# Optimization experiments

Hardware: AMD Instinct MI355X
Metric: run time of the kernel (lower is better)

## Reference

```python
import jax, jax.numpy as jnp
import numpy as np

N_NODES = 100000
N_EDGES = 1600000
IN_DIM = 10
HID = 64
OUT_DIM = 2


def _gcn_norm(edge_index, num_nodes):
    # PyG gcn_norm with add_self_loops=False, edge_weight=1
    src, dst = edge_index[0], edge_index[1]
    deg = jnp.zeros((num_nodes,), jnp.float32).at[dst].add(1.0)
    dinv = jnp.where(deg > 0, jax.lax.rsqrt(deg), 0.0)
    return dinv[src] * dinv[dst]  # [E]


def _arma_conv(x, edge_index, norm, W, V, b):
    # ARMAConv, num_stacks=1, num_layers=1 (PyG defaults):
    # out = A_norm @ (x @ W_init) + x @ V_root + b   (no internal act at T=1)
    src, dst = edge_index[0], edge_index[1]
    h = x @ W                                   # [N, F_out]
    msg = norm[:, None] * h[src]                # [E, F_out] gather
    agg = jax.ops.segment_sum(msg, dst, num_segments=x.shape[0])  # scatter-add
    return agg + x @ V + b


def setup_inputs() -> dict:
    key = jax.random.key(0)
    ks = jax.random.split(key, 9)
    x = jax.random.uniform(ks[0], (N_NODES, IN_DIM), dtype=jnp.float32)
    edge_index = jax.random.randint(ks[1], (2, N_EDGES), 0, N_NODES, dtype=jnp.int64)
    s = 0.1
    W1 = jax.random.normal(ks[2], (IN_DIM, HID), jnp.float32) * s
    V1 = jax.random.normal(ks[3], (IN_DIM, HID), jnp.float32) * s
    b1 = jnp.zeros((HID,), jnp.float32)
    W2 = jax.random.normal(ks[4], (HID, HID), jnp.float32) * s
    V2 = jax.random.normal(ks[5], (HID, HID), jnp.float32) * s
    b2 = jnp.zeros((HID,), jnp.float32)
    W3 = jax.random.normal(ks[6], (HID, OUT_DIM), jnp.float32) * s
    V3 = jax.random.normal(ks[7], (HID, OUT_DIM), jnp.float32) * s
    b3 = jnp.zeros((OUT_DIM,), jnp.float32)
    return {"x": x, "edge_index": edge_index,
            "W1": W1, "V1": V1, "b1": b1,
            "W2": W2, "V2": V2, "b2": b2,
            "W3": W3, "V3": V3, "b3": b3}


def reference(x, edge_index, W1, V1, b1, W2, V2, b2, W3, V3, b3):
    norm = _gcn_norm(edge_index, x.shape[0])
    h = jax.nn.relu(_arma_conv(x, edge_index, norm, W1, V1, b1))
    # dropout is identity at eval time
    h = jax.nn.relu(_arma_conv(h, edge_index, norm, W2, V2, b2))
    h = _arma_conv(h, edge_index, norm, W3, V3, b3)
    return jax.nn.log_softmax(h, axis=1)
```

## Files before the change

kernel.cpp:

```cpp
#include <hip/hip_runtime.h>
#include <hip/hip_fp16.h>
#include <math.h>

#define NN 100000
#define NE 1600000
#define HID 64
#define BN 128
#define NBUCK 782
#define FBCAP 2304
#define NSB 49
#define SBCAP 34816
#define CHUNK1 2048
#define NBLK1 782
#define NSLICE 16
#define SLCAP 2304
#define CSTRIDE 32
#define XPITCH 136

typedef _Float16 half8 __attribute__((ext_vector_type(8)));
typedef float floatx4 __attribute__((ext_vector_type(4)));

__device__ __forceinline__ __half2 shfl_xor_h2(__half2 v, int m) {
    unsigned int u = *(unsigned int*)&v;
    u = __shfl_xor(u, m);
    return *(__half2*)&u;
}
__device__ __forceinline__ unsigned int h2bits(__half2 v) {
    return *(unsigned int*)&v;
}


__global__ __launch_bounds__(256) void k_binA1(const int* __restrict__ src,
                                               const int* __restrict__ dst,
                                               int* __restrict__ bcur1,
                                               unsigned int* __restrict__ sbdata) {
    __shared__ unsigned int par[CHUNK1];
    __shared__ unsigned short rnk[CHUNK1];
    __shared__ unsigned char bkt[CHUNK1];
    __shared__ int hist[NSB];
    __shared__ int base[NSB];
    int tid = threadIdx.x;
    int e0 = blockIdx.x * CHUNK1;
    int m = NE - e0; if (m > CHUNK1) m = CHUNK1;
    if (tid < NSB) hist[tid] = 0;
    __syncthreads();
    for (int i = tid; i < m; i += 256) {
        int s = src[e0 + i], d = dst[e0 + i];
        int b = d >> 11;
        par[i] = (unsigned int)s | ((unsigned int)(d & 2047) << 17);
        bkt[i] = (unsigned char)b;
        rnk[i] = (unsigned short)atomicAdd(&hist[b], 1);
    }
    __syncthreads();
    if (tid < NSB) {
        int h = hist[tid];
        base[tid] = h ? atomicAdd(&bcur1[tid * CSTRIDE], h) : 0;
    }
    __syncthreads();
    for (int i = tid; i < m; i += 256) {
        int b = bkt[i];
        int pos = base[b] + rnk[i];
        if (pos < SBCAP) sbdata[(size_t)b * SBCAP + pos] = par[i];
    }
}

__global__ __launch_bounds__(256) void k_binA2(const int* __restrict__ bcur1,
                                               const unsigned int* __restrict__ sbdata,
                                               int* __restrict__ bcur2,
                                               unsigned int* __restrict__ fbdata) {
    __shared__ unsigned int par[SLCAP];
    __shared__ unsigned short rnk[SLCAP];
    __shared__ unsigned char bkt[SLCAP];
    __shared__ int hist[16];
    __shared__ int base[16];
    int tid = threadIdx.x;
    int sb = blockIdx.x >> 4, sl = blockIdx.x & 15;
    int m = bcur1[sb * CSTRIDE]; if (m > SBCAP) m = SBCAP;
    int L = (m + NSLICE - 1) >> 4;
    int lo = sl * L;
    int cnt = m - lo; if (cnt > L) cnt = L; if (cnt < 0) cnt = 0;
    if (tid < 16) hist[tid] = 0;
    __syncthreads();
    const unsigned int* sp = sbdata + (size_t)sb * SBCAP + lo;
    for (int i = tid; i < cnt; i += 256) {
        unsigned int u = sp[i];
        int dlow = (u >> 17) & 2047;
        int f = dlow >> 7;
        par[i] = (u & 0x1ffffu) | ((unsigned int)(dlow & 127) << 17);
        bkt[i] = (unsigned char)f;
        rnk[i] = (unsigned short)atomicAdd(&hist[f], 1);
    }
    __syncthreads();
    if (tid < 16) {
        int h = hist[tid];
        base[tid] = h ? atomicAdd(&bcur2[(sb * 16 + tid) * CSTRIDE], h) : 0;
    }
    __syncthreads();
    for (int i = tid; i < cnt; i += 256) {
        int f = bkt[i];
        int pos = base[f] + rnk[i];
        if (pos < FBCAP) fbdata[(size_t)(sb * 16 + f) * FBCAP + pos] = par[i];
    }
}

__global__ void k_bscan(const int* __restrict__ bcur2, int* __restrict__ ebase) {
    __shared__ int ls[16];
    int t = threadIdx.x;
    int lane = t & 63, wid = t >> 6;
    int v = 0;
    if (t < NBUCK) {
        int m = bcur2[t * CSTRIDE];
        v = (m < FBCAP) ? m : FBCAP;
    }
    int orig = v;
    for (int off = 1; off < 64; off <<= 1) {
        int u = __shfl_up(v, off);
        if (lane >= off) v += u;
    }
    if (lane == 63) ls[wid] = v;
    __syncthreads();
    if (wid == 0) {
        int w = (lane < 16) ? ls[lane] : 0;
        for (int off = 1; off < 16; off <<= 1) {
            int u = __shfl_up(w, off);
            if (lane >= off) w += u;
        }
        if (lane < 16) ls[lane] = w;
    }
    __syncthreads();
    int base = wid ? ls[wid - 1] : 0;
    int incl = base + v;
    if (t < NBUCK) ebase[t] = incl - orig;
    if (t == NBUCK - 1) ebase[NBUCK] = incl;
}

__global__ __launch_bounds__(256) void k_binB(const int* __restrict__ bcur2,
                                              const int* __restrict__ ebase,
                                              const unsigned int* __restrict__ fbdata,
                                              int* __restrict__ rp, float* __restrict__ dinv,
                                              int* __restrict__ perm) {
    __shared__ unsigned int se[FBCAP];
    __shared__ int cnt[BN];
    __shared__ int scn[BN];
    int b = blockIdx.x, tid = threadIdx.x;
    int m = bcur2[b * CSTRIDE]; if (m > FBCAP) m = FBCAP;
    int base = ebase[b];
    for (int i = tid; i < m; i += 256) se[i] = fbdata[(size_t)b * FBCAP + i];
    if (tid < BN) cnt[tid] = 0;
    __syncthreads();
    for (int i = tid; i < m; i += 256) atomicAdd(&cnt[se[i] >> 17], 1);
    __syncthreads();
    int c = (tid < BN) ? cnt[tid] : 0;
    int g = b * BN + tid;
    if (tid < BN && g < NN) dinv[g] = (c > 0) ? rsqrtf((float)c) : 0.0f;
    if (tid < BN) scn[tid] = c;
    __syncthreads();
    for (int off = 1; off < BN; off <<= 1) {
        int u = (tid >= off && tid < BN) ? scn[tid - off] : 0;
        __syncthreads();
        if (tid < BN) scn[tid] += u;
        __syncthreads();
    }
    if (tid < BN) {
        int excl = scn[tid] - c;
        if (g < NN) rp[g] = base + excl;
        cnt[tid] = excl;
    }
    if (b == NBUCK - 1 && tid == 0) rp[NN] = ebase[NBUCK];
    __syncthreads();
    for (int i = tid; i < m; i += 256) {
        unsigned int u = se[i];
        int pos = atomicAdd(&cnt[u >> 17], 1);
        perm[base + pos] = (int)(u & 0x1ffffu);
    }
}


__global__ __launch_bounds__(256) void k_l1f(
        const int* __restrict__ rp, const int* __restrict__ perm,
        const float* __restrict__ dinv, const float* __restrict__ x,
        const float* __restrict__ W, const float* __restrict__ V,
        const float* __restrict__ b, unsigned short* __restrict__ th, int N) {
    __shared__ float sW[640], sV[640];
    for (int i = threadIdx.x; i < 640; i += 256) { sW[i] = W[i]; sV[i] = V[i]; }
    __syncthreads();
    int n = (blockIdx.x * 256 + threadIdx.x) >> 4;
    if (n >= N) return;
    int sub = threadIdx.x & 15;
    int beg = rp[n], end = rp[n + 1];
    float ag[10];
#pragma unroll
    for (int k = 0; k < 10; ++k) ag[k] = 0.0f;
    for (int j = beg + sub; j < end; j += 16) {
        int s = perm[j];
        float w = dinv[s];
        const float2* xr = (const float2*)(x + (size_t)s * 10);
        float2 v0 = xr[0], v1 = xr[1], v2 = xr[2], v3 = xr[3], v4 = xr[4];
        ag[0] += w * v0.x; ag[1] += w * v0.y; ag[2] += w * v1.x; ag[3] += w * v1.y;
        ag[4] += w * v2.x; ag[5] += w * v2.y; ag[6] += w * v3.x; ag[7] += w * v3.y;
        ag[8] += w * v4.x; ag[9] += w * v4.y;
    }
#pragma unroll
    for (int mk = 1; mk <= 8; mk <<= 1) {
#pragma unroll
        for (int k = 0; k < 10; ++k) ag[k] += __shfl_xor(ag[k], mk);
    }
    float dn = dinv[n];
#pragma unroll
    for (int k = 0; k < 10; ++k) ag[k] *= dn;
    const float2* xn = (const float2*)(x + (size_t)n * 10);
    float2 x0 = xn[0], x1 = xn[1], x2 = xn[2], x3 = xn[3], x4 = xn[4];
    float xv[10] = {x0.x, x0.y, x1.x, x1.y, x2.x, x2.y, x3.x, x3.y, x4.x, x4.y};
    int f0 = sub * 4;
    float4 bb = *(const float4*)(b + f0);
    float acc[4] = {bb.x, bb.y, bb.z, bb.w};
#pragma unroll
    for (int k = 0; k < 10; ++k) {
        float4 wq = *(const float4*)&sW[k * HID + f0];
        float4 vq = *(const float4*)&sV[k * HID + f0];
        acc[0] += ag[k] * wq.x + xv[k] * vq.x;
        acc[1] += ag[k] * wq.y + xv[k] * vq.y;
        acc[2] += ag[k] * wq.z + xv[k] * vq.z;
        acc[3] += ag[k] * wq.w + xv[k] * vq.w;
    }
    __half2 lo = __floats2half2_rn(fmaxf(acc[0], 0.0f), fmaxf(acc[1], 0.0f));
    __half2 hi = __floats2half2_rn(fmaxf(acc[2], 0.0f), fmaxf(acc[3], 0.0f));
    *(uint2*)(th + (size_t)n * HID + f0) = make_uint2(h2bits(lo), h2bits(hi));
}


__global__ __launch_bounds__(256) void k_agg64h(
        const int* __restrict__ rp, const int* __restrict__ perm,
        const float* __restrict__ dinv, const unsigned short* __restrict__ th,
        unsigned short* __restrict__ aggth, int N) {
    int wid = (blockIdx.x * blockDim.x + threadIdx.x) >> 6;
    if (wid >= N) return;
    int n = __builtin_amdgcn_readfirstlane(wid);
    int lane = threadIdx.x & 63;
    int grp = lane >> 3;
    int sub = lane & 7;
    int beg = rp[n], end = rp[n + 1];
    __half2 a0 = __float2half2_rn(0.0f), a1 = a0, a2 = a0, a3 = a0;
    for (int j = beg + grp; j < end; j += 8) {
        int s = perm[j];
        __half2 w2 = __float2half2_rn(dinv[s]);
        uint4 u = *(const uint4*)(th + (size_t)s * HID + sub * 8);
        a0 = __hfma2(w2, *(__half2*)&u.x, a0);
        a1 = __hfma2(w2, *(__half2*)&u.y, a1);
        a2 = __hfma2(w2, *(__half2*)&u.z, a2);
        a3 = __hfma2(w2, *(__half2*)&u.w, a3);
    }
#pragma unroll
    for (int m = 8; m < 64; m <<= 1) {
        a0 = __hadd2(a0, shfl_xor_h2(a0, m));
        a1 = __hadd2(a1, shfl_xor_h2(a1, m));
        a2 = __hadd2(a2, shfl_xor_h2(a2, m));
        a3 = __hadd2(a3, shfl_xor_h2(a3, m));
    }
    if (grp == 0) {
        __half2 dn2 = __float2half2_rn(dinv[n]);
        uint4 o;
        o.x = h2bits(__hmul2(dn2, a0));
        o.y = h2bits(__hmul2(dn2, a1));
        o.z = h2bits(__hmul2(dn2, a2));
        o.w = h2bits(__hmul2(dn2, a3));
        *(uint4*)(aggth + (size_t)n * HID + sub * 8) = o;
    }
}

__global__ __launch_bounds__(256) void k_agg3lsm(const int* __restrict__ rp,
                                                 const int* __restrict__ perm,
                                                 const float* __restrict__ dinv,
                                                 const float2* __restrict__ h3,
                                                 const float2* __restrict__ y3,
                                                 float* __restrict__ out, int N) {
    int n = (blockIdx.x * 256 + threadIdx.x) >> 4;
    if (n >= N) return;
    int sl = threadIdx.x & 15;
    int beg = rp[n], end = rp[n + 1];
    float a0 = 0.0f, a1 = 0.0f;
    for (int j = beg + sl; j < end; j += 16) {
        int s = perm[j];
        float w = dinv[s];
        float2 hh = h3[s];
        a0 += w * hh.x;
        a1 += w * hh.y;
    }
#pragma unroll
    for (int mk = 1; mk <= 8; mk <<= 1) {
        a0 += __shfl_xor(a0, mk);
        a1 += __shfl_xor(a1, mk);
    }
    if (sl == 0) {
        float dn = dinv[n];
        float2 yy = y3[n];
        float z0 = dn * a0 + yy.x;
        float z1 = dn * a1 + yy.y;
        float m = fmaxf(z0, z1);
        float l = m + logf(expf(z0 - m) + expf(z1 - m));
        out[n * 2 + 0] = z0 - l;
        out[n * 2 + 1] = z1 - l;
    }
}


__global__ __launch_bounds__(256) void k_dense23m(
        const unsigned short* __restrict__ aggth, const unsigned short* __restrict__ th,
        const float* __restrict__ W, const float* __restrict__ V,
        const float* __restrict__ b, const float* __restrict__ W3,
        const float* __restrict__ V3, const float* __restrict__ b3,
        float2* __restrict__ h3, float2* __restrict__ y3, int N) {
    __shared__ _Float16 sX[64 * XPITCH];
    __shared__ _Float16 sWT[64 * XPITCH];
    __shared__ float sB2[64];
    __shared__ float sW3[128], sV3[128];
    int tid = threadIdx.x;
    int base = blockIdx.x * 64;
    {
        int f = tid & 63;
        int g = tid >> 6;
        const float* Wsrc = (g < 2) ? W : V;
        int kbase = (g & 1) * 32;
        int Kbase = (g < 2) ? kbase : (64 + kbase);
#pragma unroll
        for (int k2 = 0; k2 < 32; k2 += 2) {
            float w0 = Wsrc[(kbase + k2) * 64 + f];
            float w1 = Wsrc[(kbase + k2 + 1) * 64 + f];
            __half2 h = __floats2half2_rn(w0, w1);
            *(unsigned int*)&sWT[f * XPITCH + Kbase + k2] = h2bits(h);
        }
        if (tid < 64) sB2[tid] = b[tid];
        if (tid < 128) { sW3[tid] = W3[tid]; sV3[tid] = V3[tid]; }
    }
    {
        int n = tid >> 2, p = tid & 3;
        int g = base + n;
        uint4 z = make_uint4(0, 0, 0, 0);
        uint4 a0 = z, a1 = z, c0 = z, c1 = z;
        if (g < N) {
            const uint4* ap = (const uint4*)(aggth + (size_t)g * HID + p * 16);
            const uint4* cp = (const uint4*)(th + (size_t)g * HID + p * 16);
            a0 = ap[0]; a1 = ap[1];
            c0 = cp[0]; c1 = cp[1];
        }
        *(uint4*)&sX[n * XPITCH + p * 16] = a0;
        *(uint4*)&sX[n * XPITCH + p * 16 + 8] = a1;
        *(uint4*)&sX[n * XPITCH + 64 + p * 16] = c0;
        *(uint4*)&sX[n * XPITCH + 64 + p * 16 + 8] = c1;
    }
    __syncthreads();
    int lane = tid & 63;
    int wv = tid >> 6;
    int ml = lane & 15, quad = lane >> 4;
    half8 a[4];
#pragma unroll
    for (int kt = 0; kt < 4; ++kt)
        a[kt] = *(const half8*)&sX[(wv * 16 + ml) * XPITCH + kt * 32 + quad * 8];
    float p0[4] = {}, p1[4] = {}, q0[4] = {}, q1[4] = {};
#pragma unroll
    for (int c = 0; c < 4; ++c) {
        floatx4 acc = {0.0f, 0.0f, 0.0f, 0.0f};
#pragma unroll
        for (int kt = 0; kt < 4; ++kt) {
            half8 bf = *(const half8*)&sWT[(c * 16 + ml) * XPITCH + kt * 32 + quad * 8];
            acc = __builtin_amdgcn_mfma_f32_16x16x32_f16(a[kt], bf, acc, 0, 0, 0);
        }
        int col = c * 16 + ml;
        float bias = sB2[col];
        float w30 = sW3[col * 2], w31 = sW3[col * 2 + 1];
        float v30 = sV3[col * 2], v31 = sV3[col * 2 + 1];
#pragma unroll
        for (int r = 0; r < 4; ++r) {
            float t = fmaxf(acc[r] + bias, 0.0f);
            p0[r] += t * w30; p1[r] += t * w31;
            q0[r] += t * v30; q1[r] += t * v31;
        }
    }
#pragma unroll
    for (int mk = 1; mk <= 8; mk <<= 1) {
#pragma unroll
        for (int r = 0; r < 4; ++r) {
            p0[r] += __shfl_xor(p0[r], mk);
            p1[r] += __shfl_xor(p1[r], mk);
            q0[r] += __shfl_xor(q0[r], mk);
            q1[r] += __shfl_xor(q1[r], mk);
        }
    }
    if (ml == 0) {
        float b30 = b3[0], b31 = b3[1];
#pragma unroll
        for (int r = 0; r < 4; ++r) {
            int g = base + wv * 16 + quad * 4 + r;
            if (g < N) {
                h3[g] = make_float2(p0[r], p1[r]);
                y3[g] = make_float2(q0[r] + b30, q1[r] + b31);
            }
        }
    }
}


extern "C" void kernel_launch(void* const* d_in, const int* in_sizes, int n_in,
                              void* d_out, int out_size, void* d_ws, size_t ws_size,
                              hipStream_t stream) {
    const float* x  = (const float*)d_in[0];
    const int*   ei = (const int*)d_in[1];
    const int*   src = ei;
    const int*   dst = ei + NE;
    const float* W1 = (const float*)d_in[2];
    const float* V1 = (const float*)d_in[3];
    const float* b1 = (const float*)d_in[4];
    const float* W2 = (const float*)d_in[5];
    const float* V2 = (const float*)d_in[6];
    const float* b2 = (const float*)d_in[7];
    const float* W3 = (const float*)d_in[8];
    const float* V3 = (const float*)d_in[9];
    const float* b3 = (const float*)d_in[10];
    float* out = (float*)d_out;

    float* ws = (float*)d_ws;
    int*   bcur1 = (int*)ws;
    int*   bcur2 = (int*)(ws + 2048);
    int*   ebase = (int*)(ws + 27136);
    int*   rp    = (int*)(ws + 28160);
    float* dinv  = ws + 128512;
    unsigned int* sbdata = (unsigned int*)(ws + 228864);
    int*   perm  = (int*)(ws + 228864);
    unsigned int* fbdata = (unsigned int*)(ws + 1934848);
    float2* h3   = (float2*)(ws + 1934848);
    float2* y3   = (float2*)(ws + 1934848 + 2 * NN);
    unsigned short* aggth = (unsigned short*)(ws + 8334848);
    unsigned short* th    = (unsigned short*)(ws + 14734848);

    const int B = 256;

    hipMemsetAsync(bcur1, 0, 27072 * sizeof(int), stream);
    k_binA1<<<NBLK1, B, 0, stream>>>(src, dst, bcur1, sbdata);
    k_binA2<<<NSB * NSLICE, B, 0, stream>>>(bcur1, sbdata, bcur2, fbdata);
    k_bscan<<<1, 1024, 0, stream>>>(bcur2, ebase);
    k_binB<<<NBUCK, B, 0, stream>>>(bcur2, ebase, fbdata, rp, dinv, perm);

    k_l1f<<<(NN * 16 + B - 1) / B, B, 0, stream>>>(rp, perm, dinv, x, W1, V1, b1, th, NN);

    k_agg64h<<<(NN * 64 + B - 1) / B, B, 0, stream>>>(rp, perm, dinv, th, aggth, NN);
    k_dense23m<<<(NN + 63) / 64, B, 0, stream>>>(aggth, th, W2, V2, b2, W3, V3, b3,
                                                 h3, y3, NN);

    k_agg3lsm<<<(NN * 16 + B - 1) / B, B, 0, stream>>>(rp, perm, dinv,
                                                       (const float2*)h3,
                                                       (const float2*)y3, out, NN);
}
```

Baseline: 224.9 us.

## Pack quantized source dinv into perm entries and unroll 64-wide aggregation

Adds a pass that stores each edge's source dinv as a 15-bit fixed-point value in the upper bits of the perm index. The three aggregation kernels then decode the weight from the packed word instead of doing a dependent random gather of dinv[src]. The 64-wide aggregation loop is also unrolled by two to keep more loads in flight, and the binning chunk size is doubled with half as many blocks. This costs an extra full-edge kernel pass and quantizes dinv to about 6e-5 resolution, which adds precision error; values of 2 or more would overflow the 15-bit field.

Result: faster. 219.2 us (-2.5%).

```diff
diff --git a/kernel.cpp b/kernel.cpp
--- a/kernel.cpp
+++ b/kernel.cpp
@@ -10,8 +10,8 @@
 #define FBCAP 2304
 #define NSB 49
 #define SBCAP 34816
-#define CHUNK1 2048
-#define NBLK1 782
+#define CHUNK1 4096
+#define NBLK1 391
 #define NSLICE 16
 #define SLCAP 2304
 #define CSTRIDE 32
@@ -27,6 +27,9 @@
 }
 __device__ __forceinline__ unsigned int h2bits(__half2 v) {
     return *(unsigned int*)&v;
+}
+__device__ __forceinline__ float wdec(unsigned int u) {
+    return (float)(u >> 17) * 6.103515625e-05f;
 }
 
 
@@ -175,9 +178,19 @@
     }
 }
 
+__global__ __launch_bounds__(256) void k_wpack(int* __restrict__ perm,
+                                               const float* __restrict__ dinv, int E) {
+    int i = blockIdx.x * blockDim.x + threadIdx.x;
+    if (i < E) {
+        unsigned int s = (unsigned int)perm[i];
+        int q = __float2int_rn(dinv[s] * 16384.0f);
+        perm[i] = (int)(s | ((unsigned int)q << 17));
+    }
+}
+
 
 __global__ __launch_bounds__(256) void k_l1f(
-        const int* __restrict__ rp, const int* __restrict__ perm,
+        const int* __restrict__ rp, const unsigned int* __restrict__ pw,
         const float* __restrict__ dinv, const float* __restrict__ x,
         const float* __restrict__ W, const float* __restrict__ V,
         const float* __restrict__ b, unsigned short* __restrict__ th, int N) {
@@ -192,8 +205,9 @@
 #pragma unroll
     for (int k = 0; k < 10; ++k) ag[k] = 0.0f;
     for (int j = beg + sub; j < end; j += 16) {
-        int s = perm[j];
-        float w = dinv[s];
+        unsigned int pe = pw[j];
+        int s = pe & 0x1ffff;
+        float w = wdec(pe);
         const float2* xr = (const float2*)(x + (size_t)s * 10);
         float2 v0 = xr[0], v1 = xr[1], v2 = xr[2], v3 = xr[3], v4 = xr[4];
         ag[0] += w * v0.x; ag[1] += w * v0.y; ag[2] += w * v1.x; ag[3] += w * v1.y;
@@ -230,7 +244,7 @@
 
 
 __global__ __launch_bounds__(256) void k_agg64h(
-        const int* __restrict__ rp, const int* __restrict__ perm,
+        const int* __restrict__ rp, const unsigned int* __restrict__ pw,
         const float* __restrict__ dinv, const unsigned short* __restrict__ th,
         unsigned short* __restrict__ aggth, int N) {
     int wid = (blockIdx.x * blockDim.x + threadIdx.x) >> 6;
@@ -241,14 +255,32 @@
     int sub = lane & 7;
     int beg = rp[n], end = rp[n + 1];
     __half2 a0 = __float2half2_rn(0.0f), a1 = a0, a2 = a0, a3 = a0;
-    for (int j = beg + grp; j < end; j += 8) {
-        int s = perm[j];
-        __half2 w2 = __float2half2_rn(dinv[s]);
-        uint4 u = *(const uint4*)(th + (size_t)s * HID + sub * 8);
-        a0 = __hfma2(w2, *(__half2*)&u.x, a0);
-        a1 = __hfma2(w2, *(__half2*)&u.y, a1);
-        a2 = __hfma2(w2, *(__half2*)&u.z, a2);
-        a3 = __hfma2(w2, *(__half2*)&u.w, a3);
+    int j = beg + grp;
+    for (; j + 8 < end; j += 16) {
+        unsigned int pa = pw[j], pb = pw[j + 8];
+        int sa = pa & 0x1ffff, sb = pb & 0x1ffff;
+        __half2 wa = __float2half2_rn(wdec(pa));
+        __half2 wb = __float2half2_rn(wdec(pb));
+        uint4 ua = *(const uint4*)(th + (size_t)sa * HID + sub * 8);
+        uint4 ub = *(const uint4*)(th + (size_t)sb * HID + sub * 8);
+        a0 = __hfma2(wa, *(__half2*)&ua.x, a0);
+        a1 = __hfma2(wa, *(__half2*)&ua.y, a1);
+        a2 = __hfma2(wa, *(__half2*)&ua.z, a2);
+        a3 = __hfma2(wa, *(__half2*)&ua.w, a3);
+        a0 = __hfma2(wb, *(__half2*)&ub.x, a0);
+        a1 = __hfma2(wb, *(__half2*)&ub.y, a1);
+        a2 = __hfma2(wb, *(__half2*)&ub.z, a2);
+        a3 = __hfma2(wb, *(__half2*)&ub.w, a3);
+    }
+    if (j < end) {
+        unsigned int pa = pw[j];
+        int sa = pa & 0x1ffff;
+        __half2 wa = __float2half2_rn(wdec(pa));
+        uint4 ua = *(const uint4*)(th + (size_t)sa * HID + sub * 8);
+        a0 = __hfma2(wa, *(__half2*)&ua.x, a0);
+        a1 = __hfma2(wa, *(__half2*)&ua.y, a1);
+        a2 = __hfma2(wa, *(__half2*)&ua.z, a2);
+        a3 = __hfma2(wa, *(__half2*)&ua.w, a3);
     }
 #pragma unroll
     for (int m = 8; m < 64; m <<= 1) {
@@ -269,7 +301,7 @@
 }
 
 __global__ __launch_bounds__(256) void k_agg3lsm(const int* __restrict__ rp,
-                                                 const int* __restrict__ perm,
+                                                 const unsigned int* __restrict__ pw,
                                                  const float* __restrict__ dinv,
                                                  const float2* __restrict__ h3,
                                                  const float2* __restrict__ y3,
@@ -280,8 +312,9 @@
     int beg = rp[n], end = rp[n + 1];
     float a0 = 0.0f, a1 = 0.0f;
     for (int j = beg + sl; j < end; j += 16) {
-        int s = perm[j];
-        float w = dinv[s];
+        unsigned int pe = pw[j];
+        int s = pe & 0x1ffff;
+        float w = wdec(pe);
         float2 hh = h3[s];
         a0 += w * hh.x;
         a1 += w * hh.y;
@@ -439,14 +472,17 @@
     k_binA2<<<NSB * NSLICE, B, 0, stream>>>(bcur1, sbdata, bcur2, fbdata);
     k_bscan<<<1, 1024, 0, stream>>>(bcur2, ebase);
     k_binB<<<NBUCK, B, 0, stream>>>(bcur2, ebase, fbdata, rp, dinv, perm);
-
-    k_l1f<<<(NN * 16 + B - 1) / B, B, 0, stream>>>(rp, perm, dinv, x, W1, V1, b1, th, NN);
-
-    k_agg64h<<<(NN * 64 + B - 1) / B, B, 0, stream>>>(rp, perm, dinv, th, aggth, NN);
+    k_wpack<<<(NE + B - 1) / B, B, 0, stream>>>(perm, dinv, NE);
+
+    k_l1f<<<(NN * 16 + B - 1) / B, B, 0, stream>>>(rp, (const unsigned int*)perm,
+                                                   dinv, x, W1, V1, b1, th, NN);
+
+    k_agg64h<<<(NN * 64 + B - 1) / B, B, 0, stream>>>(rp, (const unsigned int*)perm,
+                                                      dinv, th, aggth, NN);
     k_dense23m<<<(NN + 63) / 64, B, 0, stream>>>(aggth, th, W2, V2, b2, W3, V3, b3,
                                                  h3, y3, NN);
 
-    k_agg3lsm<<<(NN * 16 + B - 1) / B, B, 0, stream>>>(rp, perm, dinv,
-                                                       (const float2*)h3,
+    k_agg3lsm<<<(NN * 16 + B - 1) / B, B, 0, stream>>>(rp, (const unsigned int*)perm,
+                                                       dinv, (const float2*)h3,
                                                        (const float2*)y3, out, NN);
 }
```

## Pre-scale node features by source degree norm to drop per-edge dinv gathers

Applied to the files above, without the earlier changes.

Moves the dinv[src] factor out of every edge loop by storing pre-scaled copies of node features (y = dinv*x, th2 = dinv*h, h3 scaled by dinv), so each aggregation only sums gathered rows. binB now records each edge's rank in its destination during the first atomic pass and uses a shuffle-based scan, removing the second atomic pass and the shared-memory scan loop. The 64-wide aggregation is unrolled by two, and the first binning kernel uses larger chunks with fewer blocks. In exchange it writes extra buffers (th2, y) and, because fp16 values are now scaled per node before summation, changes rounding.

Measured after the change: 212.3 us. -5.6%, faster.

```diff
diff --git a/kernel.cpp b/kernel.cpp
--- a/kernel.cpp
+++ b/kernel.cpp
@@ -10,8 +10,8 @@
 #define FBCAP 2304
 #define NSB 49
 #define SBCAP 34816
-#define CHUNK1 2048
-#define NBLK1 782
+#define CHUNK1 4096
+#define NBLK1 391
 #define NSLICE 16
 #define SLCAP 2304
 #define CSTRIDE 32
@@ -138,40 +138,64 @@
                                               const int* __restrict__ ebase,
                                               const unsigned int* __restrict__ fbdata,
                                               int* __restrict__ rp, float* __restrict__ dinv,
-                                              int* __restrict__ perm) {
+                                              int* __restrict__ perm,
+                                              const float* __restrict__ x,
+                                              float* __restrict__ y) {
     __shared__ unsigned int se[FBCAP];
+    __shared__ unsigned short rnk[FBCAP];
     __shared__ int cnt[BN];
-    __shared__ int scn[BN];
+    __shared__ int ex[BN];
+    __shared__ float sdv[BN];
+    __shared__ int wsum[2];
     int b = blockIdx.x, tid = threadIdx.x;
     int m = bcur2[b * CSTRIDE]; if (m > FBCAP) m = FBCAP;
     int base = ebase[b];
-    for (int i = tid; i < m; i += 256) se[i] = fbdata[(size_t)b * FBCAP + i];
     if (tid < BN) cnt[tid] = 0;
     __syncthreads();
-    for (int i = tid; i < m; i += 256) atomicAdd(&cnt[se[i] >> 17], 1);
-    __syncthreads();
-    int c = (tid < BN) ? cnt[tid] : 0;
-    int g = b * BN + tid;
-    if (tid < BN && g < NN) dinv[g] = (c > 0) ? rsqrtf((float)c) : 0.0f;
-    if (tid < BN) scn[tid] = c;
-    __syncthreads();
-    for (int off = 1; off < BN; off <<= 1) {
-        int u = (tid >= off && tid < BN) ? scn[tid - off] : 0;
-        __syncthreads();
-        if (tid < BN) scn[tid] += u;
-        __syncthreads();
-    }
+    for (int i = tid; i < m; i += 256) {
+        unsigned int u = fbdata[(size_t)b * FBCAP + i];
+        se[i] = u;
+        rnk[i] = (unsigned short)atomicAdd(&cnt[u >> 17], 1);
+    }
+    __syncthreads();
     if (tid < BN) {
-        int excl = scn[tid] - c;
+        int c = cnt[tid];
+        int v = c;
+        int lane = tid & 63;
+        for (int off = 1; off < 64; off <<= 1) {
+            int u = __shfl_up(v, off);
+            if (lane >= off) v += u;
+        }
+        if (lane == 63) wsum[tid >> 6] = v;
+        int g = b * BN + tid;
+        float dv = (c > 0) ? rsqrtf((float)c) : 0.0f;
+        sdv[tid] = dv;
+        if (g < NN) dinv[g] = dv;
+        cnt[tid] = v - c;
+    }
+    __syncthreads();
+    if (tid < BN) {
+        int excl = cnt[tid] + ((tid >= 64) ? wsum[0] : 0);
+        ex[tid] = excl;
+        int g = b * BN + tid;
         if (g < NN) rp[g] = base + excl;
-        cnt[tid] = excl;
     }
     if (b == NBUCK - 1 && tid == 0) rp[NN] = ebase[NBUCK];
     __syncthreads();
     for (int i = tid; i < m; i += 256) {
         unsigned int u = se[i];
-        int pos = atomicAdd(&cnt[u >> 17], 1);
-        perm[base + pos] = (int)(u & 0x1ffffu);
+        int dl = u >> 17;
+        perm[base + ex[dl] + rnk[i]] = (int)(u & 0x1ffffu);
+    }
+    {
+        int nbase = b * BN;
+        int lim = NN - nbase; if (lim > BN) lim = BN;
+        int tot = lim * 10;
+        for (int idx = tid; idx < tot; idx += 256) {
+            int nl = idx / 10;
+            int k = idx - nl * 10;
+            y[(size_t)(nbase + nl) * 10 + k] = sdv[nl] * x[(size_t)(nbase + nl) * 10 + k];
+        }
     }
 }
 
@@ -179,8 +203,10 @@
 __global__ __launch_bounds__(256) void k_l1f(
         const int* __restrict__ rp, const int* __restrict__ perm,
         const float* __restrict__ dinv, const float* __restrict__ x,
+        const float* __restrict__ y,
         const float* __restrict__ W, const float* __restrict__ V,
-        const float* __restrict__ b, unsigned short* __restrict__ th, int N) {
+        const float* __restrict__ b, unsigned short* __restrict__ th,
+        unsigned short* __restrict__ th2, int N) {
     __shared__ float sW[640], sV[640];
     for (int i = threadIdx.x; i < 640; i += 256) { sW[i] = W[i]; sV[i] = V[i]; }
     __syncthreads();
@@ -193,12 +219,11 @@
     for (int k = 0; k < 10; ++k) ag[k] = 0.0f;
     for (int j = beg + sub; j < end; j += 16) {
         int s = perm[j];
-        float w = dinv[s];
-        const float2* xr = (const float2*)(x + (size_t)s * 10);
-        float2 v0 = xr[0], v1 = xr[1], v2 = xr[2], v3 = xr[3], v4 = xr[4];
-        ag[0] += w * v0.x; ag[1] += w * v0.y; ag[2] += w * v1.x; ag[3] += w * v1.y;
-        ag[4] += w * v2.x; ag[5] += w * v2.y; ag[6] += w * v3.x; ag[7] += w * v3.y;
-        ag[8] += w * v4.x; ag[9] += w * v4.y;
+        const float2* yr = (const float2*)(y + (size_t)s * 10);
+        float2 v0 = yr[0], v1 = yr[1], v2 = yr[2], v3 = yr[3], v4 = yr[4];
+        ag[0] += v0.x; ag[1] += v0.y; ag[2] += v1.x; ag[3] += v1.y;
+        ag[4] += v2.x; ag[5] += v2.y; ag[6] += v3.x; ag[7] += v3.y;
+        ag[8] += v4.x; ag[9] += v4.y;
     }
 #pragma unroll
     for (int mk = 1; mk <= 8; mk <<= 1) {
@@ -223,15 +248,20 @@
         acc[2] += ag[k] * wq.z + xv[k] * vq.z;
         acc[3] += ag[k] * wq.w + xv[k] * vq.w;
     }
-    __half2 lo = __floats2half2_rn(fmaxf(acc[0], 0.0f), fmaxf(acc[1], 0.0f));
-    __half2 hi = __floats2half2_rn(fmaxf(acc[2], 0.0f), fmaxf(acc[3], 0.0f));
+    float t0 = fmaxf(acc[0], 0.0f), t1 = fmaxf(acc[1], 0.0f);
+    float t2 = fmaxf(acc[2], 0.0f), t3 = fmaxf(acc[3], 0.0f);
+    __half2 lo = __floats2half2_rn(t0, t1);
+    __half2 hi = __floats2half2_rn(t2, t3);
     *(uint2*)(th + (size_t)n * HID + f0) = make_uint2(h2bits(lo), h2bits(hi));
+    __half2 lo2 = __floats2half2_rn(dn * t0, dn * t1);
+    __half2 hi2 = __floats2half2_rn(dn * t2, dn * t3);
+    *(uint2*)(th2 + (size_t)n * HID + f0) = make_uint2(h2bits(lo2), h2bits(hi2));
 }
 
 
 __global__ __launch_bounds__(256) void k_agg64h(
         const int* __restrict__ rp, const int* __restrict__ perm,
-        const float* __restrict__ dinv, const unsigned short* __restrict__ th,
+        const float* __restrict__ dinv, const unsigned short* __restrict__ th2,
         unsigned short* __restrict__ aggth, int N) {
     int wid = (blockIdx.x * blockDim.x + threadIdx.x) >> 6;
     if (wid >= N) return;
@@ -241,14 +271,23 @@
     int sub = lane & 7;
     int beg = rp[n], end = rp[n + 1];
     __half2 a0 = __float2half2_rn(0.0f), a1 = a0, a2 = a0, a3 = a0;
-    for (int j = beg + grp; j < end; j += 8) {
-        int s = perm[j];
-        __half2 w2 = __float2half2_rn(dinv[s]);
-        uint4 u = *(const uint4*)(th + (size_t)s * HID + sub * 8);
-        a0 = __hfma2(w2, *(__half2*)&u.x, a0);
-        a1 = __hfma2(w2, *(__half2*)&u.y, a1);
-        a2 = __hfma2(w2, *(__half2*)&u.z, a2);
-        a3 = __hfma2(w2, *(__half2*)&u.w, a3);
+    int j = beg + grp;
+    for (; j + 8 < end; j += 16) {
+        int sa = perm[j], sb = perm[j + 8];
+        uint4 ua = *(const uint4*)(th2 + (size_t)sa * HID + sub * 8);
+        uint4 ub = *(const uint4*)(th2 + (size_t)sb * HID + sub * 8);
+        a0 = __hadd2(a0, __hadd2(*(__half2*)&ua.x, *(__half2*)&ub.x));
+        a1 = __hadd2(a1, __hadd2(*(__half2*)&ua.y, *(__half2*)&ub.y));
+        a2 = __hadd2(a2, __hadd2(*(__half2*)&ua.z, *(__half2*)&ub.z));
+        a3 = __hadd2(a3, __hadd2(*(__half2*)&ua.w, *(__half2*)&ub.w));
+    }
+    if (j < end) {
+        int sa = perm[j];
+        uint4 ua = *(const uint4*)(th2 + (size_t)sa * HID + sub * 8);
+        a0 = __hadd2(a0, *(__half2*)&ua.x);
+        a1 = __hadd2(a1, *(__half2*)&ua.y);
+        a2 = __hadd2(a2, *(__half2*)&ua.z);
+        a3 = __hadd2(a3, *(__half2*)&ua.w);
     }
 #pragma unroll
     for (int m = 8; m < 64; m <<= 1) {
@@ -281,10 +320,9 @@
     float a0 = 0.0f, a1 = 0.0f;
     for (int j = beg + sl; j < end; j += 16) {
         int s = perm[j];
-        float w = dinv[s];
         float2 hh = h3[s];
-        a0 += w * hh.x;
-        a1 += w * hh.y;
+        a0 += hh.x;
+        a1 += hh.y;
     }
 #pragma unroll
     for (int mk = 1; mk <= 8; mk <<= 1) {
@@ -309,6 +347,7 @@
         const float* __restrict__ W, const float* __restrict__ V,
         const float* __restrict__ b, const float* __restrict__ W3,
         const float* __restrict__ V3, const float* __restrict__ b3,
+        const float* __restrict__ dinv,
         float2* __restrict__ h3, float2* __restrict__ y3, int N) {
     __shared__ _Float16 sX[64 * XPITCH];
     __shared__ _Float16 sWT[64 * XPITCH];
@@ -392,7 +431,8 @@
         for (int r = 0; r < 4; ++r) {
             int g = base + wv * 16 + quad * 4 + r;
             if (g < N) {
-                h3[g] = make_float2(p0[r], p1[r]);
+                float dv = dinv[g];
+                h3[g] = make_float2(dv * p0[r], dv * p1[r]);
                 y3[g] = make_float2(q0[r] + b30, q1[r] + b31);
             }
         }
@@ -430,7 +470,9 @@
     float2* h3   = (float2*)(ws + 1934848);
     float2* y3   = (float2*)(ws + 1934848 + 2 * NN);
     unsigned short* aggth = (unsigned short*)(ws + 8334848);
+    unsigned short* th2   = (unsigned short*)(ws + 11534848);
     unsigned short* th    = (unsigned short*)(ws + 14734848);
+    float* y              = ws + 17934848;
 
     const int B = 256;
 
@@ -438,13 +480,14 @@
     k_binA1<<<NBLK1, B, 0, stream>>>(src, dst, bcur1, sbdata);
     k_binA2<<<NSB * NSLICE, B, 0, stream>>>(bcur1, sbdata, bcur2, fbdata);
     k_bscan<<<1, 1024, 0, stream>>>(bcur2, ebase);
-    k_binB<<<NBUCK, B, 0, stream>>>(bcur2, ebase, fbdata, rp, dinv, perm);
-
-    k_l1f<<<(NN * 16 + B - 1) / B, B, 0, stream>>>(rp, perm, dinv, x, W1, V1, b1, th, NN);
-
-    k_agg64h<<<(NN * 64 + B - 1) / B, B, 0, stream>>>(rp, perm, dinv, th, aggth, NN);
+    k_binB<<<NBUCK, B, 0, stream>>>(bcur2, ebase, fbdata, rp, dinv, perm, x, y);
+
+    k_l1f<<<(NN * 16 + B - 1) / B, B, 0, stream>>>(rp, perm, dinv, x, y,
+                                                   W1, V1, b1, th, th2, NN);
+
+    k_agg64h<<<(NN * 64 + B - 1) / B, B, 0, stream>>>(rp, perm, dinv, th2, aggth, NN);
     k_dense23m<<<(NN + 63) / 64, B, 0, stream>>>(aggth, th, W2, V2, b2, W3, V3, b3,
-                                                 h3, y3, NN);
+                                                 dinv, h3, y3, NN);
 
     k_agg3lsm<<<(NN * 16 + B - 1) / B, B, 0, stream>>>(rp, perm, dinv,
                                                        (const float2*)h3,
```
